# Kernel tuning notes

Measured on AMD Instinct MI355X. Metric: run time of the kernel, lower is better.

The kernel has to match this reference:

```python
import jax, jax.numpy as jnp
import numpy as np

FALSE_ALARM_COST = 1.0
MISS_CHANGE_COST = 5.0
CORRECT_REWARD = 0.1
TASK_WEIGHTS = (1.0, 0.5, 2.0)  # price_trend, volatility, regime
EPS = 1e-8
B = 8388608


def _task_loss(logits, labels):
    # logits: [B,2], labels: [B] int in {0,1}
    cost_matrix = jnp.array([[0.0, FALSE_ALARM_COST],
                             [MISS_CHANGE_COST, 0.0]], dtype=logits.dtype)
    probs = jax.nn.softmax(logits, axis=1)                       # [B,2]
    p_true = jnp.take_along_axis(probs, labels[:, None], axis=1)[:, 0]
    pred_class = jnp.argmax(probs, axis=1)                       # [B]
    base_loss = -jnp.log(p_true + EPS)                           # [B]
    cost = cost_matrix[labels, pred_class]                       # [B]
    loss = jnp.where(pred_class == labels,
                     CORRECT_REWARD * base_loss,
                     cost * base_loss)
    return loss.mean()


def setup_inputs() -> dict:
    key = jax.random.key(0)
    ks = jax.random.split(key, 6)
    return {
        "logits_a": jax.random.normal(ks[0], (B, 2), dtype=jnp.float32),
        "logits_b": jax.random.normal(ks[1], (B, 2), dtype=jnp.float32),
        "logits_c": jax.random.normal(ks[2], (B, 2), dtype=jnp.float32),
        "targets_a": jax.random.randint(ks[3], (B,), 0, 2, dtype=jnp.int32).astype(jnp.int64),
        "targets_b": jax.random.randint(ks[4], (B,), 0, 2, dtype=jnp.int32).astype(jnp.int64),
        "targets_c": jax.random.randint(ks[5], (B,), 0, 2, dtype=jnp.int32).astype(jnp.int64),
    }


def reference(logits_a, logits_b, logits_c, targets_a, targets_b, targets_c):
    la = _task_loss(logits_a, targets_a)
    lb = _task_loss(logits_b, targets_b)
    lc = _task_loss(logits_c, targets_c)
    total = TASK_WEIGHTS[0] * la + TASK_WEIGHTS[1] * lb + TASK_WEIGHTS[2] * lc
    # [loss_task_a, loss_task_b, loss_task_c, total_loss]
    return jnp.stack([la, lb, lc, total])
```

## Files before the change

kernel.cpp:

```cpp
#include <hip/hip_runtime.h>

#define TPB 256
#define NBLK 2048

__device__ __forceinline__ float elem_loss(float l0, float l1, int t) {
    float d  = l0 - l1;
    float dt = t ? -d : d;
    float base = __logf(1.0f + __expf(-dt));
    int pred = (l1 > l0) ? 1 : 0;
    float w = (pred == t) ? 0.1f : (t ? 5.0f : 1.0f);
    return w * base;
}

__global__ __launch_bounds__(TPB) void bcl_partials(
    const float4* __restrict__ la, const float4* __restrict__ lb,
    const float4* __restrict__ lc,
    const int2* __restrict__ ta, const int2* __restrict__ tb,
    const int2* __restrict__ tc,
    double* __restrict__ partials, int npairs)
{
    float sa = 0.f, sb = 0.f, sc = 0.f;
    const int stride = gridDim.x * blockDim.x;
    for (int i = blockIdx.x * blockDim.x + threadIdx.x; i < npairs; i += stride) {
        float4 a = la[i]; int2 t = ta[i];
        sa += elem_loss(a.x, a.y, t.x) + elem_loss(a.z, a.w, t.y);

        float4 b = lb[i]; int2 u = tb[i];
        sb += elem_loss(b.x, b.y, u.x) + elem_loss(b.z, b.w, u.y);

        float4 c = lc[i]; int2 v = tc[i];
        sc += elem_loss(c.x, c.y, v.x) + elem_loss(c.z, c.w, v.y);
    }

    #pragma unroll
    for (int off = 32; off > 0; off >>= 1) {
        sa += __shfl_down(sa, off, 64);
        sb += __shfl_down(sb, off, 64);
        sc += __shfl_down(sc, off, 64);
    }

    __shared__ float red[3][TPB / 64];
    const int wave = threadIdx.x >> 6;
    const int lane = threadIdx.x & 63;
    if (lane == 0) { red[0][wave] = sa; red[1][wave] = sb; red[2][wave] = sc; }
    __syncthreads();
    if (threadIdx.x == 0) {
        double pa = 0.0, pb = 0.0, pc = 0.0;
        #pragma unroll
        for (int w = 0; w < TPB / 64; ++w) {
            pa += (double)red[0][w];
            pb += (double)red[1][w];
            pc += (double)red[2][w];
        }
        partials[blockIdx.x * 3 + 0] = pa;
        partials[blockIdx.x * 3 + 1] = pb;
        partials[blockIdx.x * 3 + 2] = pc;
    }
}

__global__ __launch_bounds__(TPB) void bcl_final(
    const double* __restrict__ partials, int nblk,
    float* __restrict__ out, double invB)
{
    double sa = 0.0, sb = 0.0, sc = 0.0;
    for (int i = threadIdx.x; i < nblk; i += TPB) {
        sa += partials[i * 3 + 0];
        sb += partials[i * 3 + 1];
        sc += partials[i * 3 + 2];
    }
    #pragma unroll
    for (int off = 32; off > 0; off >>= 1) {
        sa += __shfl_down(sa, off, 64);
        sb += __shfl_down(sb, off, 64);
        sc += __shfl_down(sc, off, 64);
    }
    __shared__ double red[3][TPB / 64];
    const int wave = threadIdx.x >> 6;
    const int lane = threadIdx.x & 63;
    if (lane == 0) { red[0][wave] = sa; red[1][wave] = sb; red[2][wave] = sc; }
    __syncthreads();
    if (threadIdx.x == 0) {
        double pa = 0.0, pb = 0.0, pc = 0.0;
        #pragma unroll
        for (int w = 0; w < TPB / 64; ++w) {
            pa += red[0][w];
            pb += red[1][w];
            pc += red[2][w];
        }
        double lossA = pa * invB;
        double lossB = pb * invB;
        double lossC = pc * invB;
        double total = 1.0 * lossA + 0.5 * lossB + 2.0 * lossC;
        out[0] = (float)lossA;
        out[1] = (float)lossB;
        out[2] = (float)lossC;
        out[3] = (float)total;
    }
}

extern "C" void kernel_launch(void* const* d_in, const int* in_sizes, int n_in,
                              void* d_out, int out_size, void* d_ws, size_t ws_size,
                              hipStream_t stream) {
    const float4* la = (const float4*)d_in[0];
    const float4* lb = (const float4*)d_in[1];
    const float4* lc = (const float4*)d_in[2];
    const int2*   ta = (const int2*)d_in[3];
    const int2*   tb = (const int2*)d_in[4];
    const int2*   tc = (const int2*)d_in[5];

    const int B = in_sizes[3];
    const int npairs = B / 2;

    double* partials = (double*)d_ws;

    bcl_partials<<<NBLK, TPB, 0, stream>>>(la, lb, lc, ta, tb, tc, partials, npairs);
    bcl_final<<<1, TPB, 0, stream>>>(partials, NBLK, (float*)d_out, 1.0 / (double)B);
}
```

Before: 54.56 us.

## Fuse final reduction via last-block atomic counter and unroll loads by two

Merges the two-kernel reduction into one kernel: each block writes its partials, bumps an atomic counter, and the last block to finish reduces all partials and writes the outputs. The grid-stride loop is also unrolled by two so each thread issues twice as many independent loads before computing. This removes the second kernel launch and its gap, but adds a memset of the counter each call, plus a thread fence and atomic per block.

New measurement: 155.5 us. +184.9%, slower.

```diff
diff --git a/kernel.cpp b/kernel.cpp
--- a/kernel.cpp
+++ b/kernel.cpp
@@ -12,22 +12,39 @@
     return w * base;
 }
 
-__global__ __launch_bounds__(TPB) void bcl_partials(
+__global__ __launch_bounds__(TPB) void bcl_fused(
     const float4* __restrict__ la, const float4* __restrict__ lb,
     const float4* __restrict__ lc,
     const int2* __restrict__ ta, const int2* __restrict__ tb,
     const int2* __restrict__ tc,
-    double* __restrict__ partials, int npairs)
+    double* __restrict__ partials, unsigned int* __restrict__ counter,
+    float* __restrict__ out, int npairs, double invB)
 {
     float sa = 0.f, sb = 0.f, sc = 0.f;
     const int stride = gridDim.x * blockDim.x;
-    for (int i = blockIdx.x * blockDim.x + threadIdx.x; i < npairs; i += stride) {
+    int i = blockIdx.x * blockDim.x + threadIdx.x;
+
+    for (; i + stride < npairs; i += 2 * stride) {
+        const int j = i + stride;
+        float4 a0 = la[i]; float4 a1 = la[j];
+        float4 b0 = lb[i]; float4 b1 = lb[j];
+        float4 c0 = lc[i]; float4 c1 = lc[j];
+        int2   t0 = ta[i]; int2   t1 = ta[j];
+        int2   u0 = tb[i]; int2   u1 = tb[j];
+        int2   v0 = tc[i]; int2   v1 = tc[j];
+
+        sa += elem_loss(a0.x, a0.y, t0.x) + elem_loss(a0.z, a0.w, t0.y)
+            + elem_loss(a1.x, a1.y, t1.x) + elem_loss(a1.z, a1.w, t1.y);
+        sb += elem_loss(b0.x, b0.y, u0.x) + elem_loss(b0.z, b0.w, u0.y)
+            + elem_loss(b1.x, b1.y, u1.x) + elem_loss(b1.z, b1.w, u1.y);
+        sc += elem_loss(c0.x, c0.y, v0.x) + elem_loss(c0.z, c0.w, v0.y)
+            + elem_loss(c1.x, c1.y, v1.x) + elem_loss(c1.z, c1.w, v1.y);
+    }
+    for (; i < npairs; i += stride) {
         float4 a = la[i]; int2 t = ta[i];
         sa += elem_loss(a.x, a.y, t.x) + elem_loss(a.z, a.w, t.y);
-
         float4 b = lb[i]; int2 u = tb[i];
         sb += elem_loss(b.x, b.y, u.x) + elem_loss(b.z, b.w, u.y);
-
         float4 c = lc[i]; int2 v = tc[i];
         sc += elem_loss(c.x, c.y, v.x) + elem_loss(c.z, c.w, v.y);
     }
@@ -40,6 +57,7 @@
     }
 
     __shared__ float red[3][TPB / 64];
+    __shared__ int is_last;
     const int wave = threadIdx.x >> 6;
     const int lane = threadIdx.x & 63;
     if (lane == 0) { red[0][wave] = sa; red[1][wave] = sb; red[2][wave] = sc; }
@@ -55,46 +73,45 @@
         partials[blockIdx.x * 3 + 0] = pa;
         partials[blockIdx.x * 3 + 1] = pb;
         partials[blockIdx.x * 3 + 2] = pc;
+        __threadfence();
+        unsigned prev = atomicAdd(counter, 1u);
+        is_last = (prev == gridDim.x - 1) ? 1 : 0;
     }
-}
+    __syncthreads();
 
-__global__ __launch_bounds__(TPB) void bcl_final(
-    const double* __restrict__ partials, int nblk,
-    float* __restrict__ out, double invB)
-{
-    double sa = 0.0, sb = 0.0, sc = 0.0;
-    for (int i = threadIdx.x; i < nblk; i += TPB) {
-        sa += partials[i * 3 + 0];
-        sb += partials[i * 3 + 1];
-        sc += partials[i * 3 + 2];
-    }
-    #pragma unroll
-    for (int off = 32; off > 0; off >>= 1) {
-        sa += __shfl_down(sa, off, 64);
-        sb += __shfl_down(sb, off, 64);
-        sc += __shfl_down(sc, off, 64);
-    }
-    __shared__ double red[3][TPB / 64];
-    const int wave = threadIdx.x >> 6;
-    const int lane = threadIdx.x & 63;
-    if (lane == 0) { red[0][wave] = sa; red[1][wave] = sb; red[2][wave] = sc; }
-    __syncthreads();
-    if (threadIdx.x == 0) {
-        double pa = 0.0, pb = 0.0, pc = 0.0;
+    if (is_last) {
+        __threadfence();
+        double fa = 0.0, fb = 0.0, fc = 0.0;
+        for (int k = threadIdx.x; k < NBLK; k += TPB) {
+            fa += partials[k * 3 + 0];
+            fb += partials[k * 3 + 1];
+            fc += partials[k * 3 + 2];
+        }
         #pragma unroll
-        for (int w = 0; w < TPB / 64; ++w) {
-            pa += red[0][w];
-            pb += red[1][w];
-            pc += red[2][w];
+        for (int off = 32; off > 0; off >>= 1) {
+            fa += __shfl_down(fa, off, 64);
+            fb += __shfl_down(fb, off, 64);
+            fc += __shfl_down(fc, off, 64);
         }
-        double lossA = pa * invB;
-        double lossB = pb * invB;
-        double lossC = pc * invB;
-        double total = 1.0 * lossA + 0.5 * lossB + 2.0 * lossC;
-        out[0] = (float)lossA;
-        out[1] = (float)lossB;
-        out[2] = (float)lossC;
-        out[3] = (float)total;
+        __shared__ double red2[3][TPB / 64];
+        if (lane == 0) { red2[0][wave] = fa; red2[1][wave] = fb; red2[2][wave] = fc; }
+        __syncthreads();
+        if (threadIdx.x == 0) {
+            double pa = 0.0, pb = 0.0, pc = 0.0;
+            #pragma unroll
+            for (int w = 0; w < TPB / 64; ++w) {
+                pa += red2[0][w];
+                pb += red2[1][w];
+                pc += red2[2][w];
+            }
+            double lossA = pa * invB;
+            double lossB = pb * invB;
+            double lossC = pc * invB;
+            out[0] = (float)lossA;
+            out[1] = (float)lossB;
+            out[2] = (float)lossC;
+            out[3] = (float)(lossA + 0.5 * lossB + 2.0 * lossC);
+        }
     }
 }
 
@@ -111,8 +128,11 @@
     const int B = in_sizes[3];
     const int npairs = B / 2;
 
-    double* partials = (double*)d_ws;
+    unsigned int* counter = (unsigned int*)d_ws;
+    double* partials = (double*)((char*)d_ws + 64);
 
-    bcl_partials<<<NBLK, TPB, 0, stream>>>(la, lb, lc, ta, tb, tc, partials, npairs);
-    bcl_final<<<1, TPB, 0, stream>>>(partials, NBLK, (float*)d_out, 1.0 / (double)B);
+    hipMemsetAsync(counter, 0, sizeof(unsigned int), stream);
+    bcl_fused<<<NBLK, TPB, 0, stream>>>(la, lb, lc, ta, tb, tc,
+                                        partials, counter, (float*)d_out,
+                                        npairs, 1.0 / (double)B);
 }
```
